# Performance work log

Measured on AMD Instinct MI355X. Metric: run time of the kernel, lower is better.

The kernel has to match this reference:

```python
import jax, jax.numpy as jnp
import numpy as np

SCALE_MIN, SCALE_MAX = 0.01, 10.0
LN_EPS = 1e-5

B, KIN, H, C = 32, 6144, 512, 5


def _kaiming_uniform(k, shape):
    # torch kaiming_uniform_(a=sqrt(5)) on (out,in): bound = 1/sqrt(fan_in)
    bound = 1.0 / np.sqrt(shape[1])
    return jax.random.uniform(k, shape, minval=-bound, maxval=bound, dtype=jnp.float32)


def setup_inputs() -> dict:
    key = jax.random.key(0)
    ks = jax.random.split(key, 16)
    inp = {"x": jax.random.normal(ks[0], (B, KIN), dtype=jnp.float32)}
    dims = [(H, KIN), (H, H), (H, H)]
    for i, (o, n) in enumerate(dims):
        inp[f"w{i}"] = _kaiming_uniform(ks[1 + 3 * i], (o, n))
        inp[f"t{i}"] = jax.random.uniform(ks[2 + 3 * i], (o, n), minval=-1.0, maxval=1.0, dtype=jnp.float32)
        inp[f"s{i}"] = jax.random.uniform(ks[3 + 3 * i], (o, n), minval=-2.0, maxval=0.0, dtype=jnp.float32)
        inp[f"g{i}"] = jnp.ones((o,), jnp.float32)
        inp[f"b{i}"] = jnp.zeros((o,), jnp.float32)
    inp["cw"] = _kaiming_uniform(ks[10], (C, H))
    cbound = 1.0 / np.sqrt(H)
    inp["cb"] = jax.random.uniform(ks[11], (C,), minval=-cbound, maxval=cbound, dtype=jnp.float32)
    return inp


def _wavelet_linear(h, w, t, sr):
    # h: (B, in), params: (out, in)
    scale = SCALE_MIN + (SCALE_MAX - SCALE_MIN) * jax.nn.sigmoid(sr)
    s = (h[:, None, :] - t[None]) / (scale[None] + 1e-8)  # (B, out, in)
    psi = (1.0 - s * s) * jnp.exp(-0.5 * s * s)  # mexican hat
    return jnp.einsum('boi,oi->bo', psi, w)


def _layer_norm(h, g, b):
    m = jnp.mean(h, axis=-1, keepdims=True)
    v = jnp.mean(jnp.square(h - m), axis=-1, keepdims=True)
    return (h - m) * jax.lax.rsqrt(v + LN_EPS) * g + b


def reference(x, w0, t0, s0, g0, b0, w1, t1, s1, g1, b1, w2, t2, s2, g2, b2, cw, cb):
    h = x
    for (w, t, sr, g, b) in [(w0, t0, s0, g0, b0), (w1, t1, s1, g1, b1), (w2, t2, s2, g2, b2)]:
        h = _layer_norm(jax.nn.silu(_wavelet_linear(h, w, t, sr)), g, b)
    return h @ cw.T + cb
```

## Files before the change

### kernel.cpp

```cpp
#include <hip/hip_runtime.h>

#define LN_EPS 1e-5f
#define LOG2E 1.44269504f
#define NHALF_LOG2E (-0.72134752f)

#if __has_builtin(__builtin_amdgcn_exp2f)
#define EXP2F(x) __builtin_amdgcn_exp2f(x)
#else
#define EXP2F(x) __expf((x) * 0.69314718f)
#endif


constexpr int NBLK   = 256;
constexpr int TPB    = 512;
constexpr int NWAVES = NBLK * (TPB / 64);
constexpr int NGRP   = 8;
constexpr int GRP    = NBLK / NGRP;
constexpr int PADX   = 34;

__device__ __forceinline__ float sysld(const float* p)
{
    return __hip_atomic_load((const float*)p, __ATOMIC_RELAXED,
                             __HIP_MEMORY_SCOPE_SYSTEM);
}
__device__ __forceinline__ void sysst(float* p, float v)
{
    __hip_atomic_store(p, v, __ATOMIC_RELAXED, __HIP_MEMORY_SCOPE_SYSTEM);
}

__device__ __forceinline__ void gridbar(int* __restrict__ bar, int k)
{
    asm volatile("s_waitcnt vmcnt(0)" ::: "memory");
    __syncthreads();
    if (threadIdx.x == 0) {
        const int g = blockIdx.x >> 5;
        int* grpArr = bar + g * 32;
        int* grpRel = bar + (NGRP + g) * 32;
        int* gArr   = bar + 2 * NGRP * 32;

        int old = __hip_atomic_fetch_add(grpArr, 1, __ATOMIC_RELAXED,
                                         __HIP_MEMORY_SCOPE_AGENT);
        if (old == k * GRP - 1) {
            int o2 = __hip_atomic_fetch_add(gArr, 1, __ATOMIC_RELAXED,
                                            __HIP_MEMORY_SCOPE_AGENT);
            if (o2 == k * NGRP - 1) {
#pragma unroll
                for (int j = 0; j < NGRP; ++j)
                    __hip_atomic_store(bar + (NGRP + j) * 32, k,
                                       __ATOMIC_RELAXED, __HIP_MEMORY_SCOPE_AGENT);
            }
        }
        while (__hip_atomic_load(grpRel, __ATOMIC_RELAXED,
                                 __HIP_MEMORY_SCOPE_AGENT) < k)
            __builtin_amdgcn_s_sleep(16);
    }
    __syncthreads();
}

__device__ __forceinline__ void wav0_phase(const float* __restrict__ x,
        const float* __restrict__ w, const float* __restrict__ t,
        const float* __restrict__ s, float* __restrict__ part,
        float4* __restrict__ myPrep, float* __restrict__ xs,
        int lane, int wave)
{
    constexpr int RANGE = 192, STEPS = RANGE / 4, TPW = 8;
    const int si    = blockIdx.x >> 3;
    const int obase = (blockIdx.x & 7) * 64;
    const int ibase = si * RANGE;

    for (int b = wave; b < 32; b += 8)
        for (int i2 = lane; i2 < RANGE; i2 += 64)
            xs[i2 * PADX + b] = x[b * 6144 + ibase + i2];
    __syncthreads();

    const int p = lane & 15, g = lane >> 4;

#pragma unroll
    for (int ti = 0; ti < TPW; ++ti) {
        const int o = obase + wave * 8 + ti;
        const float* __restrict__ wp = w + (size_t)o * 6144 + ibase;
        const float* __restrict__ tp = t + (size_t)o * 6144 + ibase;
        const float* __restrict__ sp = s + (size_t)o * 6144 + ibase;

#pragma unroll
        for (int r = 0; r < RANGE / 64; ++r) {
            int il = r * 64 + lane;
            float wv = wp[il], tv = tp[il], sv = sp[il];
            float sig = __builtin_amdgcn_rcpf(1.f + EXP2F(-sv * LOG2E));
            float inv = __builtin_amdgcn_rcpf(fmaf(9.99f, sig, 0.01000001f));
            myPrep[il] = make_float4(inv, -tv * inv, wv, 0.f);
        }

        float acc0 = 0.f, acc1 = 0.f;
#pragma unroll 8
        for (int st = 0; st < STEPS; ++st) {
            float4 pr = myPrep[st * 4 + g];
            float2 xv = *(const float2*)&xs[(st * 4 + g) * PADX + 2 * p];
            float u0 = fmaf(xv.x, pr.x, pr.y);
            float u1 = fmaf(xv.y, pr.x, pr.y);
            float q0 = u0 * u0, q1 = u1 * u1;
            float e0 = EXP2F(q0 * NHALF_LOG2E);
            float e1 = EXP2F(q1 * NHALF_LOG2E);
            float pw0 = fmaf(-pr.z, q0, pr.z);
            float pw1 = fmaf(-pr.z, q1, pr.z);
            acc0 = fmaf(pw0, e0, acc0);
            acc1 = fmaf(pw1, e1, acc1);
        }

        acc0 += __shfl_down(acc0, 32); acc0 += __shfl_down(acc0, 16);
        acc1 += __shfl_down(acc1, 32); acc1 += __shfl_down(acc1, 16);
        if (lane < 16) {
            float* pp = part + (size_t)si * 16384 + o * 32 + 2 * p;
            sysst(pp, acc0); sysst(pp + 1, acc1);
        }
    }
}

__device__ __forceinline__ void wav12_phase(const float* __restrict__ hin,
        const float* __restrict__ w, const float* __restrict__ t,
        const float* __restrict__ s, float* __restrict__ part,
        float4* __restrict__ myPrep, int lane, int gw)
{
    constexpr int RANGE = 64, STEPS = RANGE / 4, TPW = 2;
    const int p = lane & 15, g = lane >> 4;

#pragma unroll
    for (int ti = 0; ti < TPW; ++ti) {
        const int tau = gw * TPW + ti;
        const int o = tau & 511, si = tau >> 9;
        const int ibase = si * RANGE;

        const float* __restrict__ wp = w + (size_t)o * 512 + ibase;
        const float* __restrict__ tp = t + (size_t)o * 512 + ibase;
        const float* __restrict__ sp = s + (size_t)o * 512 + ibase;

        {
            int il = lane;
            float wv = wp[il], tv = tp[il], sv = sp[il];
            float sig = __builtin_amdgcn_rcpf(1.f + EXP2F(-sv * LOG2E));
            float inv = __builtin_amdgcn_rcpf(fmaf(9.99f, sig, 0.01000001f));
            myPrep[il] = make_float4(inv, -tv * inv, wv, 0.f);
        }

        const float* __restrict__ hp = hin + (size_t)(ibase + g) * 32 + 2 * p;

        float acc0 = 0.f, acc1 = 0.f;
#pragma unroll 8
        for (int st = 0; st < STEPS; ++st) {
            float4 pr = myPrep[st * 4 + g];
            float x0 = sysld(hp + (size_t)st * 128);
            float x1 = sysld(hp + (size_t)st * 128 + 1);
            float u0 = fmaf(x0, pr.x, pr.y);
            float u1 = fmaf(x1, pr.x, pr.y);
            float q0 = u0 * u0, q1 = u1 * u1;
            float e0 = EXP2F(q0 * NHALF_LOG2E);
            float e1 = EXP2F(q1 * NHALF_LOG2E);
            float pw0 = fmaf(-pr.z, q0, pr.z);
            float pw1 = fmaf(-pr.z, q1, pr.z);
            acc0 = fmaf(pw0, e0, acc0);
            acc1 = fmaf(pw1, e1, acc1);
        }

        acc0 += __shfl_down(acc0, 32); acc0 += __shfl_down(acc0, 16);
        acc1 += __shfl_down(acc1, 32); acc1 += __shfl_down(acc1, 16);
        if (lane < 16) {
            float* pp = part + (size_t)si * 16384 + o * 32 + 2 * p;
            sysst(pp, acc0); sysst(pp + 1, acc1);
        }
    }
}

template<int S>
__device__ __forceinline__ void ln_phase(const float* __restrict__ part,
        const float* __restrict__ gam, const float* __restrict__ bet,
        float* __restrict__ hT, float* __restrict__ r1, float* __restrict__ r2)
{
    if (blockIdx.x < 32) {
        const int b = blockIdx.x, tid = threadIdx.x;
        float v = 0.f;
#pragma unroll
        for (int si = 0; si < S; ++si)
            v += sysld(part + (size_t)si * 16384 + tid * 32 + b);
        float a = v * __builtin_amdgcn_rcpf(1.f + EXP2F(-v * LOG2E));

        float s1 = a, s2 = a * a;
#pragma unroll
        for (int off = 32; off; off >>= 1) {
            s1 += __shfl_down(s1, off);
            s2 += __shfl_down(s2, off);
        }
        const int lane = tid & 63, wid = tid >> 6;
        if (lane == 0) { r1[wid] = s1; r2[wid] = s2; }
        __syncthreads();
        float t1 = 0.f, t2 = 0.f;
#pragma unroll
        for (int k = 0; k < 8; ++k) { t1 += r1[k]; t2 += r2[k]; }
        float m   = t1 * (1.f / 512.f);
        float var = t2 * (1.f / 512.f) - m * m;
        float r   = __builtin_amdgcn_rsqf(var + LN_EPS);
        sysst(hT + tid * 32 + b, (a - m) * r * gam[tid] + bet[tid]);
    }
}

template<int S>
__device__ __forceinline__ void cls_phase(const float* __restrict__ part,
        const float* __restrict__ gam, const float* __restrict__ bet,
        const float* __restrict__ cw, const float* __restrict__ cb,
        float* __restrict__ out, float* __restrict__ r1, float* __restrict__ r2,
        float (* __restrict__ cr)[8])
{
    if (blockIdx.x < 32) {
        const int b = blockIdx.x, tid = threadIdx.x;
        float v = 0.f;
#pragma unroll
        for (int si = 0; si < S; ++si)
            v += sysld(part + (size_t)si * 16384 + tid * 32 + b);
        float a = v * __builtin_amdgcn_rcpf(1.f + EXP2F(-v * LOG2E));

        float s1 = a, s2 = a * a;
#pragma unroll
        for (int off = 32; off; off >>= 1) {
            s1 += __shfl_down(s1, off);
            s2 += __shfl_down(s2, off);
        }
        const int lane = tid & 63, wid = tid >> 6;
        if (lane == 0) { r1[wid] = s1; r2[wid] = s2; }
        __syncthreads();
        float t1 = 0.f, t2 = 0.f;
#pragma unroll
        for (int k = 0; k < 8; ++k) { t1 += r1[k]; t2 += r2[k]; }
        float m   = t1 * (1.f / 512.f);
        float var = t2 * (1.f / 512.f) - m * m;
        float r   = __builtin_amdgcn_rsqf(var + LN_EPS);
        float hl  = (a - m) * r * gam[tid] + bet[tid];

#pragma unroll
        for (int c = 0; c < 5; ++c) {
            float pv = hl * cw[c * 512 + tid];
#pragma unroll
            for (int off = 32; off; off >>= 1) pv += __shfl_down(pv, off);
            if (lane == 0) cr[c][wid] = pv;
        }
        __syncthreads();
        if (tid < 5) {
            float sum = 0.f;
#pragma unroll
            for (int k = 0; k < 8; ++k) sum += cr[tid][k];
            out[b * 5 + tid] = sum + cb[tid];
        }
    }
}

__global__ __launch_bounds__(TPB)
void megakernel(const float* __restrict__ x,
                const float* __restrict__ w0, const float* __restrict__ t0,
                const float* __restrict__ s0, const float* __restrict__ g0,
                const float* __restrict__ b0,
                const float* __restrict__ w1, const float* __restrict__ t1,
                const float* __restrict__ s1, const float* __restrict__ g1,
                const float* __restrict__ b1,
                const float* __restrict__ w2, const float* __restrict__ t2,
                const float* __restrict__ s2, const float* __restrict__ g2,
                const float* __restrict__ b2,
                const float* __restrict__ cw, const float* __restrict__ cb,
                float* __restrict__ out,
                float* __restrict__ part, float* __restrict__ hT,
                int* __restrict__ bar)
{
    __shared__ float4 prep[8][192];
    __shared__ float  xs[192 * PADX];
    __shared__ float  r1[8], r2[8], cr[5][8];

    const int wave = threadIdx.x >> 6, lane = threadIdx.x & 63;
    const int gw = blockIdx.x * (TPB / 64) + wave;
    float4* myPrep = prep[wave];

    wav0_phase(x, w0, t0, s0, part, myPrep, xs, lane, wave);
    gridbar(bar, 1);
    ln_phase<32>(part, g0, b0, hT, r1, r2);
    gridbar(bar, 2);

    wav12_phase(hT, w1, t1, s1, part, myPrep, lane, gw);
    gridbar(bar, 3);
    ln_phase<8>(part, g1, b1, hT, r1, r2);
    gridbar(bar, 4);

    wav12_phase(hT, w2, t2, s2, part, myPrep, lane, gw);
    gridbar(bar, 5);
    cls_phase<8>(part, g2, b2, cw, cb, out, r1, r2, cr);
}

extern "C" void kernel_launch(void* const* d_in, const int* in_sizes, int n_in,
                              void* d_out, int out_size, void* d_ws, size_t ws_size,
                              hipStream_t stream)
{
    const float* x  = (const float*)d_in[0];
    const float* w0 = (const float*)d_in[1];
    const float* t0 = (const float*)d_in[2];
    const float* s0 = (const float*)d_in[3];
    const float* g0 = (const float*)d_in[4];
    const float* b0 = (const float*)d_in[5];
    const float* w1 = (const float*)d_in[6];
    const float* t1 = (const float*)d_in[7];
    const float* s1 = (const float*)d_in[8];
    const float* g1 = (const float*)d_in[9];
    const float* b1 = (const float*)d_in[10];
    const float* w2 = (const float*)d_in[11];
    const float* t2 = (const float*)d_in[12];
    const float* s2 = (const float*)d_in[13];
    const float* g2 = (const float*)d_in[14];
    const float* b2 = (const float*)d_in[15];
    const float* cw = (const float*)d_in[16];
    const float* cb = (const float*)d_in[17];
    float* out = (float*)d_out;

    float* part = (float*)d_ws;
    float* hT   = part + 32 * 16384;
    int*   bar  = (int*)(hT + 16384);

    hipMemsetAsync(bar, 0, 4096, stream);

    void* args[] = { (void*)&x,
                     (void*)&w0, (void*)&t0, (void*)&s0, (void*)&g0, (void*)&b0,
                     (void*)&w1, (void*)&t1, (void*)&s1, (void*)&g1, (void*)&b1,
                     (void*)&w2, (void*)&t2, (void*)&s2, (void*)&g2, (void*)&b2,
                     (void*)&cw, (void*)&cb, (void*)&out,
                     (void*)&part, (void*)&hT, (void*)&bar };

    hipLaunchKernel((const void*)megakernel, dim3(NBLK), dim3(TPB),
                    args, 0, stream);
}
```

Baseline: 190.6 us.

## Double grid size, prefetch layer weights across grid barriers, vectorize atomic exchanges

The persistent megakernel grid goes from 256 to 512 blocks, with 16 barrier groups, so each wave handles fewer output rows per phase and more waves hide latency. Weight, center and scale values for the next wavelet row are loaded into registers before they are needed. For layers 1 and 2 they are fetched before the preceding grid barrier, so that load latency overlaps the barrier wait and the LayerNorm phase. Paired partial-sum stores and hidden-state loads use 64-bit system-scope atomics, and the barrier spin sleep is shortened. The risks are that all 512 blocks must be co-resident for the grid barrier to work, and that register pressure rises under the new launch bound.

```diff
diff --git a/kernel.cpp b/kernel.cpp
--- a/kernel.cpp
+++ b/kernel.cpp
@@ -11,21 +11,32 @@
 #endif
 
 
-constexpr int NBLK   = 256;
+constexpr int NBLK   = 512;
 constexpr int TPB    = 512;
 constexpr int NWAVES = NBLK * (TPB / 64);
-constexpr int NGRP   = 8;
+constexpr int NGRP   = 16;
 constexpr int GRP    = NBLK / NGRP;
 constexpr int PADX   = 34;
 
 __device__ __forceinline__ float sysld(const float* p)
 {
-    return __hip_atomic_load((const float*)p, __ATOMIC_RELAXED,
-                             __HIP_MEMORY_SCOPE_SYSTEM);
+    return __hip_atomic_load(p, __ATOMIC_RELAXED, __HIP_MEMORY_SCOPE_SYSTEM);
 }
 __device__ __forceinline__ void sysst(float* p, float v)
 {
     __hip_atomic_store(p, v, __ATOMIC_RELAXED, __HIP_MEMORY_SCOPE_SYSTEM);
+}
+__device__ __forceinline__ float2 sysld2(const float* p)
+{
+    unsigned long long v = __hip_atomic_load((const unsigned long long*)p,
+        __ATOMIC_RELAXED, __HIP_MEMORY_SCOPE_SYSTEM);
+    union { unsigned long long u; float2 f; } c; c.u = v; return c.f;
+}
+__device__ __forceinline__ void sysst2(float* p, float a, float b)
+{
+    union { unsigned long long u; float2 f; } c; c.f = make_float2(a, b);
+    __hip_atomic_store((unsigned long long*)p, c.u, __ATOMIC_RELAXED,
+                       __HIP_MEMORY_SCOPE_SYSTEM);
 }
 
 __device__ __forceinline__ void gridbar(int* __restrict__ bar, int k)
@@ -52,7 +63,7 @@
         }
         while (__hip_atomic_load(grpRel, __ATOMIC_RELAXED,
                                  __HIP_MEMORY_SCOPE_AGENT) < k)
-            __builtin_amdgcn_s_sleep(16);
+            __builtin_amdgcn_s_sleep(8);
     }
     __syncthreads();
 }
@@ -63,9 +74,9 @@
         float4* __restrict__ myPrep, float* __restrict__ xs,
         int lane, int wave)
 {
-    constexpr int RANGE = 192, STEPS = RANGE / 4, TPW = 8;
-    const int si    = blockIdx.x >> 3;
-    const int obase = (blockIdx.x & 7) * 64;
+    constexpr int RANGE = 192, STEPS = RANGE / 4, TPW = 4;
+    const int si    = blockIdx.x >> 4;
+    const int obase = (blockIdx.x & 15) * 32;
     const int ibase = si * RANGE;
 
     for (int b = wave; b < 32; b += 8)
@@ -74,21 +85,36 @@
     __syncthreads();
 
     const int p = lane & 15, g = lane >> 4;
+    const int o0 = obase + wave * TPW;
+    const float* __restrict__ wp = w + (size_t)o0 * 6144 + ibase;
+    const float* __restrict__ tp = t + (size_t)o0 * 6144 + ibase;
+    const float* __restrict__ sp = s + (size_t)o0 * 6144 + ibase;
+
+    float fw[3], ft[3], fs[3];
+#pragma unroll
+    for (int r = 0; r < 3; ++r) {
+        int il = r * 64 + lane;
+        fw[r] = wp[il]; ft[r] = tp[il]; fs[r] = sp[il];
+    }
 
 #pragma unroll
     for (int ti = 0; ti < TPW; ++ti) {
-        const int o = obase + wave * 8 + ti;
-        const float* __restrict__ wp = w + (size_t)o * 6144 + ibase;
-        const float* __restrict__ tp = t + (size_t)o * 6144 + ibase;
-        const float* __restrict__ sp = s + (size_t)o * 6144 + ibase;
-
-#pragma unroll
-        for (int r = 0; r < RANGE / 64; ++r) {
+#pragma unroll
+        for (int r = 0; r < 3; ++r) {
             int il = r * 64 + lane;
-            float wv = wp[il], tv = tp[il], sv = sp[il];
-            float sig = __builtin_amdgcn_rcpf(1.f + EXP2F(-sv * LOG2E));
+            float sig = __builtin_amdgcn_rcpf(1.f + EXP2F(-fs[r] * LOG2E));
             float inv = __builtin_amdgcn_rcpf(fmaf(9.99f, sig, 0.01000001f));
-            myPrep[il] = make_float4(inv, -tv * inv, wv, 0.f);
+            myPrep[il] = make_float4(inv, -ft[r] * inv, fw[r], 0.f);
+        }
+        if (ti + 1 < TPW) {
+            const float* wpn = wp + (size_t)(ti + 1) * 6144;
+            const float* tpn = tp + (size_t)(ti + 1) * 6144;
+            const float* spn = sp + (size_t)(ti + 1) * 6144;
+#pragma unroll
+            for (int r = 0; r < 3; ++r) {
+                int il = r * 64 + lane;
+                fw[r] = wpn[il]; ft[r] = tpn[il]; fs[r] = spn[il];
+            }
         }
 
         float acc0 = 0.f, acc1 = 0.f;
@@ -110,64 +136,49 @@
         acc0 += __shfl_down(acc0, 32); acc0 += __shfl_down(acc0, 16);
         acc1 += __shfl_down(acc1, 32); acc1 += __shfl_down(acc1, 16);
         if (lane < 16) {
-            float* pp = part + (size_t)si * 16384 + o * 32 + 2 * p;
-            sysst(pp, acc0); sysst(pp + 1, acc1);
+            const int o = o0 + ti;
+            sysst2(part + (size_t)si * 16384 + o * 32 + 2 * p, acc0, acc1);
         }
     }
 }
 
 __device__ __forceinline__ void wav12_phase(const float* __restrict__ hin,
-        const float* __restrict__ w, const float* __restrict__ t,
-        const float* __restrict__ s, float* __restrict__ part,
-        float4* __restrict__ myPrep, int lane, int gw)
-{
-    constexpr int RANGE = 64, STEPS = RANGE / 4, TPW = 2;
+        float* __restrict__ part, float4* __restrict__ myPrep,
+        int lane, int gw, float fw, float ft, float fs)
+{
+    constexpr int STEPS = 16;
     const int p = lane & 15, g = lane >> 4;
-
-#pragma unroll
-    for (int ti = 0; ti < TPW; ++ti) {
-        const int tau = gw * TPW + ti;
-        const int o = tau & 511, si = tau >> 9;
-        const int ibase = si * RANGE;
-
-        const float* __restrict__ wp = w + (size_t)o * 512 + ibase;
-        const float* __restrict__ tp = t + (size_t)o * 512 + ibase;
-        const float* __restrict__ sp = s + (size_t)o * 512 + ibase;
-
-        {
-            int il = lane;
-            float wv = wp[il], tv = tp[il], sv = sp[il];
-            float sig = __builtin_amdgcn_rcpf(1.f + EXP2F(-sv * LOG2E));
-            float inv = __builtin_amdgcn_rcpf(fmaf(9.99f, sig, 0.01000001f));
-            myPrep[il] = make_float4(inv, -tv * inv, wv, 0.f);
-        }
-
-        const float* __restrict__ hp = hin + (size_t)(ibase + g) * 32 + 2 * p;
-
-        float acc0 = 0.f, acc1 = 0.f;
+    const int o = gw & 511, si = gw >> 9;
+    const int ibase = si * 64;
+
+    {
+        float sig = __builtin_amdgcn_rcpf(1.f + EXP2F(-fs * LOG2E));
+        float inv = __builtin_amdgcn_rcpf(fmaf(9.99f, sig, 0.01000001f));
+        myPrep[lane] = make_float4(inv, -ft * inv, fw, 0.f);
+    }
+
+    const float* __restrict__ hp = hin + (size_t)(ibase + g) * 32 + 2 * p;
+
+    float acc0 = 0.f, acc1 = 0.f;
 #pragma unroll 8
-        for (int st = 0; st < STEPS; ++st) {
-            float4 pr = myPrep[st * 4 + g];
-            float x0 = sysld(hp + (size_t)st * 128);
-            float x1 = sysld(hp + (size_t)st * 128 + 1);
-            float u0 = fmaf(x0, pr.x, pr.y);
-            float u1 = fmaf(x1, pr.x, pr.y);
-            float q0 = u0 * u0, q1 = u1 * u1;
-            float e0 = EXP2F(q0 * NHALF_LOG2E);
-            float e1 = EXP2F(q1 * NHALF_LOG2E);
-            float pw0 = fmaf(-pr.z, q0, pr.z);
-            float pw1 = fmaf(-pr.z, q1, pr.z);
-            acc0 = fmaf(pw0, e0, acc0);
-            acc1 = fmaf(pw1, e1, acc1);
-        }
-
-        acc0 += __shfl_down(acc0, 32); acc0 += __shfl_down(acc0, 16);
-        acc1 += __shfl_down(acc1, 32); acc1 += __shfl_down(acc1, 16);
-        if (lane < 16) {
-            float* pp = part + (size_t)si * 16384 + o * 32 + 2 * p;
-            sysst(pp, acc0); sysst(pp + 1, acc1);
-        }
-    }
+    for (int st = 0; st < STEPS; ++st) {
+        float4 pr = myPrep[st * 4 + g];
+        float2 xv = sysld2(hp + (size_t)st * 128);
+        float u0 = fmaf(xv.x, pr.x, pr.y);
+        float u1 = fmaf(xv.y, pr.x, pr.y);
+        float q0 = u0 * u0, q1 = u1 * u1;
+        float e0 = EXP2F(q0 * NHALF_LOG2E);
+        float e1 = EXP2F(q1 * NHALF_LOG2E);
+        float pw0 = fmaf(-pr.z, q0, pr.z);
+        float pw1 = fmaf(-pr.z, q1, pr.z);
+        acc0 = fmaf(pw0, e0, acc0);
+        acc1 = fmaf(pw1, e1, acc1);
+    }
+
+    acc0 += __shfl_down(acc0, 32); acc0 += __shfl_down(acc0, 16);
+    acc1 += __shfl_down(acc1, 32); acc1 += __shfl_down(acc1, 16);
+    if (lane < 16)
+        sysst2(part + (size_t)si * 16384 + o * 32 + 2 * p, acc0, acc1);
 }
 
 template<int S>
@@ -251,7 +262,7 @@
     }
 }
 
-__global__ __launch_bounds__(TPB)
+__global__ __launch_bounds__(TPB, 4)
 void megakernel(const float* __restrict__ x,
                 const float* __restrict__ w0, const float* __restrict__ t0,
                 const float* __restrict__ s0, const float* __restrict__ g0,
@@ -276,16 +287,20 @@
     float4* myPrep = prep[wave];
 
     wav0_phase(x, w0, t0, s0, part, myPrep, xs, lane, wave);
+    const int o1 = gw & 511, si1 = gw >> 9;
+    const size_t off1 = (size_t)o1 * 512 + si1 * 64 + lane;
+    float fw1 = w1[off1], ft1 = t1[off1], fs1 = s1[off1];
     gridbar(bar, 1);
     ln_phase<32>(part, g0, b0, hT, r1, r2);
     gridbar(bar, 2);
 
-    wav12_phase(hT, w1, t1, s1, part, myPrep, lane, gw);
+    wav12_phase(hT, part, myPrep, lane, gw, fw1, ft1, fs1);
+    float fw2 = w2[off1], ft2 = t2[off1], fs2 = s2[off1];
     gridbar(bar, 3);
     ln_phase<8>(part, g1, b1, hT, r1, r2);
     gridbar(bar, 4);
 
-    wav12_phase(hT, w2, t2, s2, part, myPrep, lane, gw);
+    wav12_phase(hT, part, myPrep, lane, gw, fw2, ft2, fs2);
     gridbar(bar, 5);
     cls_phase<8>(part, g2, b2, cw, cb, out, r1, r2, cr);
 }
@@ -318,7 +333,7 @@
     float* hT   = part + 32 * 16384;
     int*   bar  = (int*)(hT + 16384);
 
-    hipMemsetAsync(bar, 0, 4096, stream);
+    hipMemsetAsync(bar, 0, 8192, stream);
 
     void* args[] = { (void*)&x,
                      (void*)&w0, (void*)&t0, (void*)&s0, (void*)&g0, (void*)&b0,
```

After: 179.2 us. 1.06x faster.
